# Performance work log

Hardware: AMD Instinct MI355X
Metric: run time of the kernel (lower is better)

## Reference

```python
import jax, jax.numpy as jnp
import numpy as np

INPUT_SIZE = 768
HIDDEN = [512, 256, 128]
LATENT = 32
NUM_LEVELS = 3
CODEBOOK_SIZE = 256
BATCH = 131072


def _init_linear(key, d_in, d_out):
    kw, kb = jax.random.split(key)
    lim = 1.0 / np.sqrt(d_in)
    W = jax.random.uniform(kw, (d_in, d_out), jnp.float32, -lim, lim)
    b = jax.random.uniform(kb, (d_out,), jnp.float32, -lim, lim)
    return W, b


def setup_inputs() -> dict:
    key = jax.random.key(0)
    keys = jax.random.split(key, 16)
    inp = {"x": jax.random.normal(keys[0], (BATCH, INPUT_SIZE), jnp.float32)}
    enc_dims = [INPUT_SIZE] + HIDDEN + [LATENT]          # 768->512->256->128->32
    dec_dims = [LATENT] + HIDDEN[::-1] + [INPUT_SIZE]     # 32->128->256->512->768
    for i in range(4):
        W, b = _init_linear(keys[1 + i], enc_dims[i], enc_dims[i + 1])
        inp[f"enc_W{i}"], inp[f"enc_b{i}"] = W, b
        W, b = _init_linear(keys[6 + i], dec_dims[i], dec_dims[i + 1])
        inp[f"dec_W{i}"], inp[f"dec_b{i}"] = W, b
    inp["codebooks"] = jax.random.normal(keys[12], (NUM_LEVELS, CODEBOOK_SIZE, LATENT), jnp.float32)
    return inp


def _mlp(x, Ws, bs):
    # Linear -> ReLU (-> Dropout p=0, identity) between layers, final layer linear.
    n = len(Ws)
    for i in range(n):
        x = x @ Ws[i] + bs[i]
        if i < n - 1:
            x = jax.nn.relu(x)
    return x


def _quantize(z, codebooks):
    # Residual vector quantization over NUM_LEVELS codebooks.
    L, K, D = codebooks.shape
    r = z
    idxs, rs, es = [], [], []
    for l in range(L):
        c = codebooks[l]                                  # [K, D]
        # squared-distance argmin (same argmin as cdist)
        d = jnp.sum(r * r, axis=-1, keepdims=True) - 2.0 * (r @ c.T) + jnp.sum(c * c, axis=-1)
        idx = jnp.argmin(d, axis=-1)                      # [B]
        e = c[idx]                                        # [B, D] gather
        idxs.append(idx)
        rs.append(r)
        es.append(e)
        r = r - e
    quantized = jnp.stack(idxs, axis=1)                   # [B, L] int codes
    r_stack = jnp.stack(rs, axis=1)                       # [B, L, D] residual inputs per level
    e_stack = jnp.stack(es, axis=1)                       # [B, L, D] selected embeddings
    sum_e = jnp.sum(e_stack, axis=1)                      # [B, D]
    # straight-through estimator
    z_hat = z + jax.lax.stop_gradient(sum_e - z)
    counts = jnp.sum(jax.nn.one_hot(quantized, K, dtype=jnp.float32), axis=0)  # [L, K] usage
    return quantized, r_stack, e_stack, z_hat, counts


def reference(x,
              enc_W0, enc_b0, enc_W1, enc_b1, enc_W2, enc_b2, enc_W3, enc_b3,
              dec_W0, dec_b0, dec_W1, dec_b1, dec_W2, dec_b2, dec_W3, dec_b3,
              codebooks):
    encoded = _mlp(x, [enc_W0, enc_W1, enc_W2, enc_W3], [enc_b0, enc_b1, enc_b2, enc_b3])
    quantized, r, e, z_hat, counts = _quantize(encoded, codebooks)
    decoded = _mlp(z_hat, [dec_W0, dec_W1, dec_W2, dec_W3], [dec_b0, dec_b1, dec_b2, dec_b3])
    return decoded, r, e, counts, quantized
```

## Files before the change

### kernel.cpp

```cpp
#include <hip/hip_runtime.h>
#include <hip/hip_bf16.h>
#include <cfloat>

#define B_TOTAL 131072
#define IN_DIM  768
#define NLEV    3
#define KCODE   256

typedef unsigned short u16;
typedef unsigned int   u32;
typedef __attribute__((ext_vector_type(8))) short bf16x8;
typedef __attribute__((ext_vector_type(4))) float f32x4;

#define GLOAD_LDS(g, l)                                                        \
    __builtin_amdgcn_global_load_lds(                                          \
        (const __attribute__((address_space(1))) u32*)(g),                     \
        (__attribute__((address_space(3))) u32*)(l), 16, 0, 0)

#define SWZ(row) ((((row) >> 1) & 3u) << 4)

__device__ __forceinline__ u16 f2bf(float x) {
    union { __hip_bfloat16 h; u16 u; } c;
    c.h = __float2bfloat16(x);
    return c.u;
}
__device__ __forceinline__ float bf2f(u32 lo16) {
    union { u32 v; float f; } c;
    c.v = lo16 << 16;
    return c.f;
}
__device__ __forceinline__ u32 pack2(float a, float b) {
    return (u32)f2bf(a) | ((u32)f2bf(b) << 16);
}

template<int K, int N, bool AF32, bool RELU, bool OUTF32>
__global__ __launch_bounds__(512)
void gemm_mfma(const void* __restrict__ A_, const u16* __restrict__ Wt,
               const float* __restrict__ bias, void* __restrict__ C_)
{
    constexpr int NK  = K / 32;
    constexpr int NCB = N / 128;
    __shared__ u16 As[3][8192];
    __shared__ u16 Bs[3][4096];

    const int tid  = threadIdx.x;
    const int lane = tid & 63;
    const int wid  = tid >> 6;
    const int wrow = wid >> 1;
    const int wcol = wid & 1;

    const u32 nwg  = gridDim.x;
    const u32 orig = blockIdx.x;
    const u32 xcd = orig & 7u, q8 = nwg >> 3, r8 = nwg & 7u;
    const u32 wg = (xcd < r8 ? xcd * (q8 + 1) : r8 * (q8 + 1) + (xcd - r8) * q8)
                 + (orig >> 3);
    const int col0 = (int)(wg % NCB) * 128;
    const int row0 = (int)(wg / NCB) * 256;

    const u16*   Ab = (const u16*)A_;
    const float* Af = (const float*)A_;

    f32x4 acc[4][4];
    #pragma unroll
    for (int i = 0; i < 4; ++i)
        #pragma unroll
        for (int j = 0; j < 4; ++j) acc[i][j] = (f32x4){0.f, 0.f, 0.f, 0.f};

    auto stage_B = [&](u16* dstbase, const u16* src) {
        const u32 o   = (u32)(tid * 16);
        const u32 row = o >> 6;
        const u32 cbs = (o & 63u) ^ SWZ(row);
        GLOAD_LDS((const char*)(src + (size_t)row * K) + cbs,
                  dstbase + wid * 512);
    };
    auto stage_A = [&](u16* dstbase, const u16* src) {
        #pragma unroll
        for (int i = 0; i < 2; ++i) {
            const u32 o   = (u32)(i * 8192 + tid * 16);
            const u32 row = o >> 6;
            const u32 cbs = (o & 63u) ^ SWZ(row);
            GLOAD_LDS((const char*)(src + (size_t)row * K) + cbs,
                      dstbase + (i * 4096 + wid * 512));
        }
    };
    auto stage_tile = [&](int buf, int kt) {
        stage_B(&Bs[buf][0], Wt + (size_t)col0 * K + kt * 32);
        stage_A(&As[buf][0], Ab + (size_t)row0 * K + kt * 32);
    };

    auto compute = [&](int buf) {
        const char* Ab8 = (const char*)&As[buf][0];
        const char* Bb8 = (const char*)&Bs[buf][0];
        const int kb = (lane >> 4) * 16;
        bf16x8 af[4], bf[4];
        #pragma unroll
        for (int mf = 0; mf < 4; ++mf) {
            const int r = wrow * 64 + mf * 16 + (lane & 15);
            af[mf] = *(const bf16x8*)(Ab8 + r * 64 + (kb ^ SWZ(r)));
        }
        #pragma unroll
        for (int nf = 0; nf < 4; ++nf) {
            const int r = wcol * 64 + nf * 16 + (lane & 15);
            bf[nf] = *(const bf16x8*)(Bb8 + r * 64 + (kb ^ SWZ(r)));
        }
        __builtin_amdgcn_s_setprio(1);
        #pragma unroll
        for (int mf = 0; mf < 4; ++mf)
            #pragma unroll
            for (int nf = 0; nf < 4; ++nf)
                acc[mf][nf] = __builtin_amdgcn_mfma_f32_16x16x32_bf16(
                    af[mf], bf[nf], acc[mf][nf], 0, 0, 0);
        __builtin_amdgcn_s_setprio(0);
    };

    if constexpr (AF32) {
        float4 fa[4];
        auto loadA = [&](int kt) {
            const int row = tid >> 1;
            const int ce0 = (tid & 1) * 16;
            const float* s = &Af[(size_t)(row0 + row) * K + kt * 32 + ce0];
            fa[0] = *(const float4*)(s + 0);
            fa[1] = *(const float4*)(s + 4);
            fa[2] = *(const float4*)(s + 8);
            fa[3] = *(const float4*)(s + 12);
        };
        auto writeA = [&](int buf) {
            const int row = tid >> 1;
            const u32 cb0 = (u32)((tid & 1) * 32);
            const u32 sw  = SWZ(row);
            char* lb = (char*)&As[buf][0] + row * 64;
            *(uint4*)(lb + ((cb0 + 0) ^ sw)) = make_uint4(
                pack2(fa[0].x, fa[0].y), pack2(fa[0].z, fa[0].w),
                pack2(fa[1].x, fa[1].y), pack2(fa[1].z, fa[1].w));
            *(uint4*)(lb + ((cb0 + 16) ^ sw)) = make_uint4(
                pack2(fa[2].x, fa[2].y), pack2(fa[2].z, fa[2].w),
                pack2(fa[3].x, fa[3].y), pack2(fa[3].z, fa[3].w));
        };

        loadA(0);
        stage_B(&Bs[0][0], Wt + (size_t)col0 * K);
        writeA(0);
        if (NK > 1) {
            loadA(1);
            stage_B(&Bs[1][0], Wt + (size_t)col0 * K + 32);
        }

        #pragma unroll 1
        for (int kt = 0; kt < NK; ++kt) {
            if (kt == NK - 1) asm volatile("s_waitcnt vmcnt(0) lgkmcnt(0)");
            else              asm volatile("s_waitcnt vmcnt(5) lgkmcnt(0)");
            __builtin_amdgcn_sched_barrier(0);
            __builtin_amdgcn_s_barrier();
            __builtin_amdgcn_sched_barrier(0);
            if (kt + 1 < NK) writeA((kt + 1) % 3);
            if (kt + 2 < NK) {
                loadA(kt + 2);
                stage_B(&Bs[(kt + 2) % 3][0],
                        Wt + (size_t)col0 * K + (kt + 2) * 32);
            }
            compute(kt % 3);
        }
    } else {
        stage_tile(0, 0);
        if (NK > 1) stage_tile(1, 1);
        int cb_ = 0, sb_ = 2;
        #pragma unroll 1
        for (int kt = 0; kt < NK; ++kt) {
            if (kt == NK - 1) asm volatile("s_waitcnt vmcnt(0)");
            else              asm volatile("s_waitcnt vmcnt(3)");
            __builtin_amdgcn_sched_barrier(0);
            __builtin_amdgcn_s_barrier();
            __builtin_amdgcn_sched_barrier(0);
            if (kt + 2 < NK) stage_tile(sb_, kt + 2);
            compute(cb_);
            cb_ = (cb_ == 2) ? 0 : cb_ + 1;
            sb_ = (sb_ == 2) ? 0 : sb_ + 1;
        }
    }

    #pragma unroll
    for (int nf = 0; nf < 4; ++nf) {
        const int col = col0 + wcol * 64 + nf * 16 + (lane & 15);
        const float bv = bias[col];
        #pragma unroll
        for (int mf = 0; mf < 4; ++mf) {
            const int rbase = row0 + wrow * 64 + mf * 16 + (lane >> 4) * 4;
            #pragma unroll
            for (int r = 0; r < 4; ++r) {
                float o = acc[mf][nf][r] + bv;
                if (RELU) o = fmaxf(o, 0.f);
                if constexpr (OUTF32)
                    ((float*)C_)[(size_t)(rbase + r) * N + col] = o;
                else
                    ((u16*)C_)[(size_t)(rbase + r) * N + col] = f2bf(o);
            }
        }
    }
}

template<int K, int N>
__global__ __launch_bounds__(256)
void wcvt(const float* __restrict__ W, u16* __restrict__ Wt)
{
    const int idx = blockIdx.x * 256 + threadIdx.x;
    const int k = idx / N, n = idx - k * N;
    Wt[(size_t)n * K + k] = f2bf(W[idx]);
}

__global__ __launch_bounds__(256)
void vq_kernel(const u16* __restrict__ h3, const float* __restrict__ eW3,
               const float* __restrict__ eb3, const float* __restrict__ cb,
               float* __restrict__ r_out, float* __restrict__ e_out,
               float* __restrict__ q_out, u16* __restrict__ se_ws,
               u32* __restrict__ ghist, size_t grow_base)
{
    __shared__ float W3[128 * 32];
    __shared__ float ebv[32];
    __shared__ float clds[256 * 36];
    __shared__ float cc2[256];
    __shared__ u32   lh[NLEV * KCODE];

    const int tid = threadIdx.x;
    const size_t lrow = (size_t)blockIdx.x * 256 + tid;
    const size_t grow = grow_base + lrow;

    for (int i = tid; i < 128 * 32; i += 256) W3[i] = eW3[i];
    if (tid < 32) ebv[tid] = eb3[tid];
    for (int i = tid; i < NLEV * KCODE; i += 256) lh[i] = 0;
    __syncthreads();

    float r[32];
    #pragma unroll
    for (int j = 0; j < 32; ++j) r[j] = ebv[j];
    {
        const u32* hrow = (const u32*)h3 + lrow * 64;
        #pragma unroll 2
        for (int k2 = 0; k2 < 64; ++k2) {
            const u32 v = hrow[k2];
            const float x0 = bf2f(v & 0xffffu), x1 = bf2f(v >> 16);
            const float* w0 = &W3[(2 * k2) * 32];
            const float* w1 = &W3[(2 * k2 + 1) * 32];
            #pragma unroll
            for (int j4 = 0; j4 < 8; ++j4) {
                const float4 a = *(const float4*)&w0[4 * j4];
                const float4 b = *(const float4*)&w1[4 * j4];
                r[4*j4+0] = fmaf(x1, b.x, fmaf(x0, a.x, r[4*j4+0]));
                r[4*j4+1] = fmaf(x1, b.y, fmaf(x0, a.y, r[4*j4+1]));
                r[4*j4+2] = fmaf(x1, b.z, fmaf(x0, a.z, r[4*j4+2]));
                r[4*j4+3] = fmaf(x1, b.w, fmaf(x0, a.w, r[4*j4+3]));
            }
        }
    }

    float z0[32];
    #pragma unroll
    for (int j = 0; j < 32; ++j) z0[j] = r[j];

    #pragma unroll 1
    for (int l = 0; l < NLEV; ++l) {
        __syncthreads();
        {
            const float* cl = cb + ((size_t)l * KCODE + tid) * 32;
            float s = 0.f;
            #pragma unroll
            for (int m = 0; m < 8; ++m) {
                const float4 v = *(const float4*)&cl[4 * m];
                *(float4*)&clds[tid * 36 + 4 * m] = v;
                s = fmaf(v.x, v.x, s); s = fmaf(v.y, v.y, s);
                s = fmaf(v.z, v.z, s); s = fmaf(v.w, v.w, s);
            }
            cc2[tid] = -0.5f * s;
        }
        __syncthreads();

        float best = -FLT_MAX;
        int   bidx = 0;
        #pragma unroll 1
        for (int k = 0; k < KCODE; ++k) {
            const float* ck = &clds[k * 36];
            float d0 = 0.f, d1 = 0.f, d2 = 0.f, d3 = 0.f;
            #pragma unroll
            for (int m = 0; m < 8; m += 4) {
                const float4 v0 = *(const float4*)&ck[4 * (m + 0)];
                const float4 v1 = *(const float4*)&ck[4 * (m + 1)];
                const float4 v2 = *(const float4*)&ck[4 * (m + 2)];
                const float4 v3 = *(const float4*)&ck[4 * (m + 3)];
                d0 = fmaf(r[4*m+0],  v0.x, d0); d0 = fmaf(r[4*m+1],  v0.y, d0);
                d0 = fmaf(r[4*m+2],  v0.z, d0); d0 = fmaf(r[4*m+3],  v0.w, d0);
                d1 = fmaf(r[4*m+4],  v1.x, d1); d1 = fmaf(r[4*m+5],  v1.y, d1);
                d1 = fmaf(r[4*m+6],  v1.z, d1); d1 = fmaf(r[4*m+7],  v1.w, d1);
                d2 = fmaf(r[4*m+8],  v2.x, d2); d2 = fmaf(r[4*m+9],  v2.y, d2);
                d2 = fmaf(r[4*m+10], v2.z, d2); d2 = fmaf(r[4*m+11], v2.w, d2);
                d3 = fmaf(r[4*m+12], v3.x, d3); d3 = fmaf(r[4*m+13], v3.y, d3);
                d3 = fmaf(r[4*m+14], v3.z, d3); d3 = fmaf(r[4*m+15], v3.w, d3);
            }
            const float s = ((d0 + d1) + (d2 + d3)) + cc2[k];
            if (s > best) { best = s; bidx = k; }
        }

        const size_t base = (grow * NLEV + l) * 32;
        const float* ce = &clds[bidx * 36];
        #pragma unroll
        for (int m = 0; m < 8; ++m) {
            const float4 ev = *(const float4*)&ce[4 * m];
            *(float4*)&r_out[base + 4 * m] =
                make_float4(r[4*m+0], r[4*m+1], r[4*m+2], r[4*m+3]);
            *(float4*)&e_out[base + 4 * m] = ev;
            r[4*m+0] -= ev.x; r[4*m+1] -= ev.y;
            r[4*m+2] -= ev.z; r[4*m+3] -= ev.w;
        }
        q_out[grow * NLEV + l] = (float)bidx;
        atomicAdd(&lh[l * KCODE + bidx], 1u);
    }

    u32* sed = (u32*)se_ws + lrow * 16;
    #pragma unroll
    for (int m = 0; m < 16; ++m)
        sed[m] = pack2(z0[2*m] - r[2*m], z0[2*m+1] - r[2*m+1]);

    __syncthreads();
    for (int i = tid; i < NLEV * KCODE; i += 256)
        if (lh[i]) atomicAdd(&ghist[i], lh[i]);
}

__global__ void zero_hist(u32* h) {
    if (threadIdx.x < NLEV * KCODE) h[threadIdx.x] = 0;
}
__global__ void counts_fin(const u32* __restrict__ g, float* __restrict__ o) {
    if (threadIdx.x < NLEV * KCODE) o[threadIdx.x] = (float)g[threadIdx.x];
}

__global__ __launch_bounds__(256)
void counts_k(const float* __restrict__ q, float* __restrict__ cnt)
{
    const int l = blockIdx.x >> 8;
    const int k = blockIdx.x & 255;
    const float pat = (float)k;
    int c = 0;
    for (int i = threadIdx.x; i < B_TOTAL; i += 256)
        c += (q[(size_t)i * NLEV + l] == pat) ? 1 : 0;
    __shared__ int red[256];
    red[threadIdx.x] = c;
    __syncthreads();
    for (int s = 128; s > 0; s >>= 1) {
        if (threadIdx.x < s) red[threadIdx.x] += red[threadIdx.x + s];
        __syncthreads();
    }
    if (threadIdx.x == 0)
        cnt[blockIdx.x] = (float)red[0];
}

template<int K, int N, bool RELU, bool AGLOBAL>
static __device__ __forceinline__
void layer16(const float* __restrict__ A, size_t grow0,
             const float* __restrict__ W, const float* __restrict__ bias,
             float* __restrict__ C)
{
    constexpr int QPT = N / 128;
    const int tr = threadIdx.x >> 5;
    const int tc = threadIdx.x & 31;
    float acc[2][QPT * 4];
    #pragma unroll
    for (int i = 0; i < 2; ++i)
        #pragma unroll
        for (int j = 0; j < QPT * 4; ++j) acc[i][j] = 0.f;
    #pragma unroll 2
    for (int k0 = 0; k0 < K; k0 += 4) {
        float4 av[2];
        #pragma unroll
        for (int i = 0; i < 2; ++i) {
            if (AGLOBAL)
                av[i] = *(const float4*)&A[(grow0 + tr * 2 + i) * (size_t)K + k0];
            else
                av[i] = *(const float4*)&A[(tr * 2 + i) * K + k0];
        }
        #pragma unroll
        for (int kk = 0; kk < 4; ++kk) {
            #pragma unroll
            for (int q = 0; q < QPT; ++q) {
                const float4 w4 = *(const float4*)&W[(size_t)(k0 + kk) * N + 4 * (tc + 32 * q)];
                #pragma unroll
                for (int i = 0; i < 2; ++i) {
                    const float a = ((const float*)&av[i])[kk];
                    acc[i][4*q+0] = fmaf(a, w4.x, acc[i][4*q+0]);
                    acc[i][4*q+1] = fmaf(a, w4.y, acc[i][4*q+1]);
                    acc[i][4*q+2] = fmaf(a, w4.z, acc[i][4*q+2]);
                    acc[i][4*q+3] = fmaf(a, w4.w, acc[i][4*q+3]);
                }
            }
        }
    }
    #pragma unroll
    for (int q = 0; q < QPT; ++q) {
        const float4 b4 = *(const float4*)&bias[4 * (tc + 32 * q)];
        #pragma unroll
        for (int i = 0; i < 2; ++i) {
            float4 o;
            o.x = acc[i][4*q+0] + b4.x; o.y = acc[i][4*q+1] + b4.y;
            o.z = acc[i][4*q+2] + b4.z; o.w = acc[i][4*q+3] + b4.w;
            if (RELU) {
                o.x = fmaxf(o.x, 0.f); o.y = fmaxf(o.y, 0.f);
                o.z = fmaxf(o.z, 0.f); o.w = fmaxf(o.w, 0.f);
            }
            *(float4*)&C[(tr * 2 + i) * N + 4 * (tc + 32 * q)] = o;
        }
    }
}

static __device__ __forceinline__
void layer_final16(const float* __restrict__ A, const float* __restrict__ W,
                   const float* __restrict__ bias, float* __restrict__ Cg, size_t grow0)
{
    constexpr int QPT = 6;
    const int tr = threadIdx.x >> 5;
    const int tc = threadIdx.x & 31;
    float acc[2][QPT * 4];
    #pragma unroll
    for (int i = 0; i < 2; ++i)
        #pragma unroll
        for (int j = 0; j < QPT * 4; ++j) acc[i][j] = 0.f;
    #pragma unroll 2
    for (int k0 = 0; k0 < 512; k0 += 4) {
        float4 av[2];
        #pragma unroll
        for (int i = 0; i < 2; ++i)
            av[i] = *(const float4*)&A[(tr * 2 + i) * 512 + k0];
        #pragma unroll
        for (int kk = 0; kk < 4; ++kk) {
            #pragma unroll
            for (int q = 0; q < QPT; ++q) {
                const float4 w4 = *(const float4*)&W[(size_t)(k0 + kk) * 768 + 4 * (tc + 32 * q)];
                #pragma unroll
                for (int i = 0; i < 2; ++i) {
                    const float a = ((const float*)&av[i])[kk];
                    acc[i][4*q+0] = fmaf(a, w4.x, acc[i][4*q+0]);
                    acc[i][4*q+1] = fmaf(a, w4.y, acc[i][4*q+1]);
                    acc[i][4*q+2] = fmaf(a, w4.z, acc[i][4*q+2]);
                    acc[i][4*q+3] = fmaf(a, w4.w, acc[i][4*q+3]);
                }
            }
        }
    }
    #pragma unroll
    for (int q = 0; q < QPT; ++q) {
        const float4 b4 = *(const float4*)&bias[4 * (tc + 32 * q)];
        #pragma unroll
        for (int i = 0; i < 2; ++i) {
            float4 s;
            s.x = acc[i][4*q+0] + b4.x; s.y = acc[i][4*q+1] + b4.y;
            s.z = acc[i][4*q+2] + b4.z; s.w = acc[i][4*q+3] + b4.w;
            *(float4*)&Cg[(grow0 + tr * 2 + i) * (size_t)768 + 4 * (tc + 32 * q)] = s;
        }
    }
}

static __device__ __forceinline__
void layer_narrow16(const float* __restrict__ A, const float* __restrict__ W,
                    const float* __restrict__ bias, float* __restrict__ Z)
{
    const int row = threadIdx.x >> 4;
    const int g   = threadIdx.x & 15;
    float a0 = 0.f, a1 = 0.f;
    #pragma unroll 4
    for (int k0 = 0; k0 < 128; k0 += 4) {
        const float4 av = *(const float4*)&A[row * 128 + k0];
        #pragma unroll
        for (int kk = 0; kk < 4; ++kk) {
            const float2 w2 = *(const float2*)&W[(k0 + kk) * 32 + 2 * g];
            const float a = ((const float*)&av)[kk];
            a0 = fmaf(a, w2.x, a0);
            a1 = fmaf(a, w2.y, a1);
        }
    }
    Z[row * 36 + 2 * g + 0] = a0 + bias[2 * g + 0];
    Z[row * 36 + 2 * g + 1] = a1 + bias[2 * g + 1];
}

__global__ __launch_bounds__(256)
void enc_vq_kernel(const float* __restrict__ x,
                   const float* __restrict__ eW0, const float* __restrict__ eb0,
                   const float* __restrict__ eW1, const float* __restrict__ eb1,
                   const float* __restrict__ eW2, const float* __restrict__ eb2,
                   const float* __restrict__ eW3, const float* __restrict__ eb3,
                   const float* __restrict__ cb,
                   float* __restrict__ r_out, float* __restrict__ e_out,
                   float* __restrict__ q_out)
{
    __shared__ __align__(16) char smem[59648];
    float* h1   = (float*)(smem);
    float* h2   = (float*)(smem + 32768);
    float* h3   = (float*)(smem + 49152);
    float* z    = (float*)(smem + 57344);
    float* clds = (float*)(smem);
    float* cc   = (float*)(smem + 36864);

    const size_t grow0 = (size_t)blockIdx.x * 16;
    layer16<768, 512, true, true >(x,  grow0, eW0, eb0, h1);
    __syncthreads();
    layer16<512, 256, true, false>(h1, 0,     eW1, eb1, h2);
    __syncthreads();
    layer16<256, 128, true, false>(h2, 0,     eW2, eb2, h3);
    __syncthreads();
    layer_narrow16(h3, eW3, eb3, z);

    const int row = threadIdx.x >> 4;
    const int g   = threadIdx.x & 15;
    const size_t grow = grow0 + row;

    #pragma unroll 1
    for (int l = 0; l < NLEV; ++l) {
        __syncthreads();
        {
            const float* cl = cb + (size_t)l * KCODE * 32;
            const int t = threadIdx.x;
            float s = 0.f;
            #pragma unroll
            for (int m = 0; m < 8; ++m) {
                const float4 v = *(const float4*)&cl[t * 32 + 4 * m];
                *(float4*)&clds[t * 36 + 4 * m] = v;
                s = fmaf(v.x, v.x, s); s = fmaf(v.y, v.y, s);
                s = fmaf(v.z, v.z, s); s = fmaf(v.w, v.w, s);
            }
            cc[t] = s;
        }
        __syncthreads();

        float r[32];
        #pragma unroll
        for (int m = 0; m < 8; ++m) {
            const float4 v = *(const float4*)&z[row * 36 + 4 * m];
            r[4*m+0] = v.x; r[4*m+1] = v.y; r[4*m+2] = v.z; r[4*m+3] = v.w;
        }
        float rr = 0.f;
        #pragma unroll
        for (int j = 0; j < 32; ++j) rr = fmaf(r[j], r[j], rr);

        float best = FLT_MAX;
        int   bidx = 0x7fffffff;
        #pragma unroll 1
        for (int t = 0; t < 16; ++t) {
            const int k = g + 16 * t;
            const float* ck = &clds[k * 36];
            float d0 = 0.f, d1 = 0.f, d2 = 0.f, d3 = 0.f;
            #pragma unroll
            for (int m = 0; m < 8; m += 4) {
                const float4 v0 = *(const float4*)&ck[4 * (m + 0)];
                const float4 v1 = *(const float4*)&ck[4 * (m + 1)];
                const float4 v2 = *(const float4*)&ck[4 * (m + 2)];
                const float4 v3 = *(const float4*)&ck[4 * (m + 3)];
                d0 = fmaf(r[4*m+0],  v0.x, d0); d0 = fmaf(r[4*m+1],  v0.y, d0);
                d0 = fmaf(r[4*m+2],  v0.z, d0); d0 = fmaf(r[4*m+3],  v0.w, d0);
                d1 = fmaf(r[4*m+4],  v1.x, d1); d1 = fmaf(r[4*m+5],  v1.y, d1);
                d1 = fmaf(r[4*m+6],  v1.z, d1); d1 = fmaf(r[4*m+7],  v1.w, d1);
                d2 = fmaf(r[4*m+8],  v2.x, d2); d2 = fmaf(r[4*m+9],  v2.y, d2);
                d2 = fmaf(r[4*m+10], v2.z, d2); d2 = fmaf(r[4*m+11], v2.w, d2);
                d3 = fmaf(r[4*m+12], v3.x, d3); d3 = fmaf(r[4*m+13], v3.y, d3);
                d3 = fmaf(r[4*m+14], v3.z, d3); d3 = fmaf(r[4*m+15], v3.w, d3);
            }
            const float dot = (d0 + d1) + (d2 + d3);
            const float d = (rr - 2.f * dot) + cc[k];
            if (d < best || (d == best && k < bidx)) { best = d; bidx = k; }
        }
        #pragma unroll
        for (int off = 1; off < 16; off <<= 1) {
            const float ob = __shfl_xor(best, off);
            const int   oi = __shfl_xor(bidx, off);
            if (ob < best || (ob == best && oi < bidx)) { best = ob; bidx = oi; }
        }

        const float evx = clds[bidx * 36 + 2 * g + 0];
        const float evy = clds[bidx * 36 + 2 * g + 1];
        *(float2*)&r_out[(grow * NLEV + l) * 32 + 2 * g] = make_float2(r[2*g], r[2*g+1]);
        *(float2*)&e_out[(grow * NLEV + l) * 32 + 2 * g] = make_float2(evx, evy);
        if (g == 0) q_out[grow * NLEV + l] = (float)bidx;
        z[row * 36 + 2 * g + 0] = r[2 * g + 0] - evx;
        z[row * 36 + 2 * g + 1] = r[2 * g + 1] - evy;
    }
}

__global__ __launch_bounds__(256)
void dec_kernel(const float* __restrict__ e_in,
                const float* __restrict__ dW0, const float* __restrict__ db0,
                const float* __restrict__ dW1, const float* __restrict__ db1,
                const float* __restrict__ dW2, const float* __restrict__ db2,
                const float* __restrict__ dW3, const float* __restrict__ db3,
                float* __restrict__ dec_out)
{
    __shared__ __align__(16) char smem[59392];
    float* h3 = (float*)(smem);
    float* h2 = (float*)(smem + 32768);
    float* h1 = (float*)(smem + 49152);
    float* se = (float*)(smem + 57344);

    const size_t grow0 = (size_t)blockIdx.x * 16;
    const int row = threadIdx.x >> 4;
    const int g   = threadIdx.x & 15;
    {
        const size_t base = ((grow0 + row) * NLEV) * 32 + 2 * g;
        float s0 = 0.f, s1 = 0.f;
        #pragma unroll
        for (int l = 0; l < NLEV; ++l) {
            const float2 v = *(const float2*)&e_in[base + l * 32];
            s0 += v.x; s1 += v.y;
        }
        se[row * 32 + 2 * g + 0] = s0;
        se[row * 32 + 2 * g + 1] = s1;
    }
    __syncthreads();
    layer16<32,  128, true, false>(se, 0, dW0, db0, h1);
    __syncthreads();
    layer16<128, 256, true, false>(h1, 0, dW1, db1, h2);
    __syncthreads();
    layer16<256, 512, true, false>(h2, 0, dW2, db2, h3);
    __syncthreads();
    layer_final16(h3, dW3, db3, dec_out, grow0);
}

extern "C" void kernel_launch(void* const* d_in, const int* in_sizes, int n_in,
                              void* d_out, int out_size, void* d_ws, size_t ws_size,
                              hipStream_t stream)
{
    (void)in_sizes; (void)n_in; (void)out_size;
    const float* x  = (const float*)d_in[0];
    const float* cb = (const float*)d_in[17];
    const float *eW[4], *eb[4], *dW[4], *db[4];
    for (int i = 0; i < 4; ++i) {
        eW[i] = (const float*)d_in[1 + 4 * i];
        eb[i] = (const float*)d_in[2 + 4 * i];
        dW[i] = (const float*)d_in[3 + 4 * i];
        db[i] = (const float*)d_in[4 + 4 * i];
    }

    float* out = (float*)d_out;
    const size_t OFF_R = (size_t)B_TOTAL * IN_DIM;
    const size_t OFF_E = OFF_R + (size_t)B_TOTAL * NLEV * 32;
    const size_t OFF_C = OFF_E + (size_t)B_TOTAL * NLEV * 32;
    const size_t OFF_Q = OFF_C + (size_t)NLEV * KCODE;

    const size_t WTB = 2236416;
    size_t R = 0;
    for (size_t cand = 131072; cand >= 2048; cand >>= 1)
        if (WTB + cand * 3648 + 4096 <= ws_size) { R = cand; break; }

    if (R && d_ws) {
        u16* Wp   = (u16*)d_ws;
        u16* WtE0 = Wp;
        u16* WtE1 = WtE0 + 393216;
        u16* WtE2 = WtE1 + 131072;
        u16* WtD0 = WtE2 + 32768;
        u16* WtD1 = WtD0 + 4096;
        u16* WtD2 = WtD1 + 32768;
        u16* WtD3 = WtD2 + 131072;
        u16* h1   = WtD3 + 393216;
        u16* h2   = h1 + R * 512;
        u16* h3   = h2 + R * 256;
        u16* se   = h3 + R * 128;
        u16* d1   = se + R * 32;
        u16* d2   = d1 + R * 128;
        u16* d3   = d2 + R * 256;
        u32* ghist = (u32*)(d3 + R * 512);

        wcvt<768, 512><<<dim3((768 * 512) / 256), 256, 0, stream>>>(eW[0], WtE0);
        wcvt<512, 256><<<dim3((512 * 256) / 256), 256, 0, stream>>>(eW[1], WtE1);
        wcvt<256, 128><<<dim3((256 * 128) / 256), 256, 0, stream>>>(eW[2], WtE2);
        wcvt<32,  128><<<dim3((32 * 128) / 256),  256, 0, stream>>>(dW[0], WtD0);
        wcvt<128, 256><<<dim3((128 * 256) / 256), 256, 0, stream>>>(dW[1], WtD1);
        wcvt<256, 512><<<dim3((256 * 512) / 256), 256, 0, stream>>>(dW[2], WtD2);
        wcvt<512, 768><<<dim3((512 * 768) / 256), 256, 0, stream>>>(dW[3], WtD3);
        zero_hist<<<1, 768, 0, stream>>>(ghist);

        const int nch = B_TOTAL / (int)R;
        const int MB2 = (int)R / 256;
        for (int c = 0; c < nch; ++c) {
            const size_t rb = (size_t)c * R;
            gemm_mfma<768, 512, true,  true,  false><<<dim3(4 * MB2), 512, 0, stream>>>(
                x + rb * 768, WtE0, eb[0], h1);
            gemm_mfma<512, 256, false, true,  false><<<dim3(2 * MB2), 512, 0, stream>>>(
                h1, WtE1, eb[1], h2);
            gemm_mfma<256, 128, false, true,  false><<<dim3(1 * MB2), 512, 0, stream>>>(
                h2, WtE2, eb[2], h3);
            vq_kernel<<<dim3((int)R / 256), 256, 0, stream>>>(
                h3, eW[3], eb[3], cb,
                out + OFF_R, out + OFF_E, out + OFF_Q, se, ghist, rb);
            gemm_mfma<32,  128, false, true,  false><<<dim3(1 * MB2), 512, 0, stream>>>(
                se, WtD0, db[0], d1);
            gemm_mfma<128, 256, false, true,  false><<<dim3(2 * MB2), 512, 0, stream>>>(
                d1, WtD1, db[1], d2);
            gemm_mfma<256, 512, false, true,  false><<<dim3(4 * MB2), 512, 0, stream>>>(
                d2, WtD2, db[2], d3);
            gemm_mfma<512, 768, false, false, true ><<<dim3(6 * MB2), 512, 0, stream>>>(
                d3, WtD3, db[3], out + rb * 768);
        }
        counts_fin<<<1, 768, 0, stream>>>(ghist, out + OFF_C);
    } else {
        enc_vq_kernel<<<dim3(B_TOTAL / 16), 256, 0, stream>>>(
            x, eW[0], eb[0], eW[1], eb[1], eW[2], eb[2], eW[3], eb[3], cb,
            out + OFF_R, out + OFF_E, out + OFF_Q);
        counts_k<<<dim3(NLEV * KCODE), 256, 0, stream>>>(out + OFF_Q, out + OFF_C);
        dec_kernel<<<dim3(B_TOTAL / 16), 256, 0, stream>>>(
            out + OFF_E, dW[0], db[0], dW[1], db[1], dW[2], db[2], dW[3], db[3], out);
    }
}
```

Before: 852.0 us.

## Add 256x256-tile MFMA GEMM for wide layers and merge weight prep kernels

Adds a GEMM variant with 256x256 output tiles (each wave computes 128x64) and uses it for the encoder 512->256 layer and the three wider decoder layers. This halves the block count and raises operand reuse per LDS load. It also merges the seven weight-transpose kernels and the histogram zeroing into one prep launch to cut launch overhead. The cost is higher register pressure (32 accumulators per lane) and fewer blocks per layer, which may reduce occupancy and tail balance.

New measurement: 878.3 us. 1.03x slower.

```diff
diff --git a/kernel.cpp b/kernel.cpp
--- a/kernel.cpp
+++ b/kernel.cpp
@@ -31,6 +31,12 @@
 }
 __device__ __forceinline__ u32 pack2(float a, float b) {
     return (u32)f2bf(a) | ((u32)f2bf(b) << 16);
+}
+
+__device__ __forceinline__ u32 xcd_swizzle(u32 orig, u32 nwg) {
+    const u32 xcd = orig & 7u, q8 = nwg >> 3, r8 = nwg & 7u;
+    return (xcd < r8 ? xcd * (q8 + 1) : r8 * (q8 + 1) + (xcd - r8) * q8)
+           + (orig >> 3);
 }
 
 template<int K, int N, bool AF32, bool RELU, bool OUTF32>
@@ -49,11 +55,7 @@
     const int wrow = wid >> 1;
     const int wcol = wid & 1;
 
-    const u32 nwg  = gridDim.x;
-    const u32 orig = blockIdx.x;
-    const u32 xcd = orig & 7u, q8 = nwg >> 3, r8 = nwg & 7u;
-    const u32 wg = (xcd < r8 ? xcd * (q8 + 1) : r8 * (q8 + 1) + (xcd - r8) * q8)
-                 + (orig >> 3);
+    const u32 wg = xcd_swizzle(blockIdx.x, gridDim.x);
     const int col0 = (int)(wg % NCB) * 128;
     const int row0 = (int)(wg / NCB) * 256;
 
@@ -198,13 +200,142 @@
     }
 }
 
-template<int K, int N>
+template<int K, int N, bool RELU, bool OUTF32>
+__global__ __launch_bounds__(512)
+void gemm_mfma256(const u16* __restrict__ Ab, const u16* __restrict__ Wt,
+                  const float* __restrict__ bias, void* __restrict__ C_)
+{
+    constexpr int NK  = K / 32;
+    constexpr int NCB = N / 256;
+    __shared__ u16 As[3][8192];
+    __shared__ u16 Bs[3][8192];
+
+    const int tid  = threadIdx.x;
+    const int lane = tid & 63;
+    const int wid  = tid >> 6;
+    const int wrow = wid >> 2;
+    const int wcol = wid & 3;
+
+    const u32 wg = xcd_swizzle(blockIdx.x, gridDim.x);
+    const int col0 = (int)(wg % NCB) * 256;
+    const int row0 = (int)(wg / NCB) * 256;
+
+    f32x4 acc[8][4];
+    #pragma unroll
+    for (int i = 0; i < 8; ++i)
+        #pragma unroll
+        for (int j = 0; j < 4; ++j) acc[i][j] = (f32x4){0.f, 0.f, 0.f, 0.f};
+
+    auto stage_one = [&](u16* dstbase, const u16* src) {
+        #pragma unroll
+        for (int i = 0; i < 2; ++i) {
+            const u32 o   = (u32)(i * 8192 + tid * 16);
+            const u32 row = o >> 6;
+            const u32 cbs = (o & 63u) ^ SWZ(row);
+            GLOAD_LDS((const char*)(src + (size_t)row * K) + cbs,
+                      dstbase + (i * 4096 + wid * 512));
+        }
+    };
+    auto stage_tile = [&](int buf, int kt) {
+        stage_one(&Bs[buf][0], Wt + (size_t)col0 * K + kt * 32);
+        stage_one(&As[buf][0], Ab + (size_t)row0 * K + kt * 32);
+    };
+
+    auto compute = [&](int buf) {
+        const char* Ab8 = (const char*)&As[buf][0];
+        const char* Bb8 = (const char*)&Bs[buf][0];
+        const int kb = (lane >> 4) * 16;
+        bf16x8 af[8], bf[4];
+        #pragma unroll
+        for (int mf = 0; mf < 8; ++mf) {
+            const int r = wrow * 128 + mf * 16 + (lane & 15);
+            af[mf] = *(const bf16x8*)(Ab8 + r * 64 + (kb ^ SWZ(r)));
+        }
+        #pragma unroll
+        for (int nf = 0; nf < 4; ++nf) {
+            const int r = wcol * 64 + nf * 16 + (lane & 15);
+            bf[nf] = *(const bf16x8*)(Bb8 + r * 64 + (kb ^ SWZ(r)));
+        }
+        __builtin_amdgcn_s_setprio(1);
+        #pragma unroll
+        for (int mf = 0; mf < 8; ++mf)
+            #pragma unroll
+            for (int nf = 0; nf < 4; ++nf)
+                acc[mf][nf] = __builtin_amdgcn_mfma_f32_16x16x32_bf16(
+                    af[mf], bf[nf], acc[mf][nf], 0, 0, 0);
+        __builtin_amdgcn_s_setprio(0);
+    };
+
+    stage_tile(0, 0);
+    if (NK > 1) stage_tile(1, 1);
+    int cb_ = 0, sb_ = 2;
+    #pragma unroll 1
+    for (int kt = 0; kt < NK; ++kt) {
+        if (kt == NK - 1) asm volatile("s_waitcnt vmcnt(0)");
+        else              asm volatile("s_waitcnt vmcnt(4)");
+        __builtin_amdgcn_sched_barrier(0);
+        __builtin_amdgcn_s_barrier();
+        __builtin_amdgcn_sched_barrier(0);
+        if (kt + 2 < NK) stage_tile(sb_, kt + 2);
+        compute(cb_);
+        cb_ = (cb_ == 2) ? 0 : cb_ + 1;
+        sb_ = (sb_ == 2) ? 0 : sb_ + 1;
+    }
+
+    #pragma unroll
+    for (int nf = 0; nf < 4; ++nf) {
+        const int col = col0 + wcol * 64 + nf * 16 + (lane & 15);
+        const float bv = bias[col];
+        #pragma unroll
+        for (int mf = 0; mf < 8; ++mf) {
+            const int rbase = row0 + wrow * 128 + mf * 16 + (lane >> 4) * 4;
+            #pragma unroll
+            for (int r = 0; r < 4; ++r) {
+                float o = acc[mf][nf][r] + bv;
+                if (RELU) o = fmaxf(o, 0.f);
+                if constexpr (OUTF32)
+                    ((float*)C_)[(size_t)(rbase + r) * N + col] = o;
+                else
+                    ((u16*)C_)[(size_t)(rbase + r) * N + col] = f2bf(o);
+            }
+        }
+    }
+}
+
 __global__ __launch_bounds__(256)
-void wcvt(const float* __restrict__ W, u16* __restrict__ Wt)
-{
-    const int idx = blockIdx.x * 256 + threadIdx.x;
-    const int k = idx / N, n = idx - k * N;
-    Wt[(size_t)n * K + k] = f2bf(W[idx]);
+void prep(const float* __restrict__ eW0, const float* __restrict__ eW1,
+          const float* __restrict__ eW2, const float* __restrict__ dW0,
+          const float* __restrict__ dW1, const float* __restrict__ dW2,
+          const float* __restrict__ dW3,
+          u16* __restrict__ tE0, u16* __restrict__ tE1, u16* __restrict__ tE2,
+          u16* __restrict__ tD0, u16* __restrict__ tD1, u16* __restrict__ tD2,
+          u16* __restrict__ tD3, u32* __restrict__ ghist)
+{
+    const int i = blockIdx.x * 256 + threadIdx.x;
+    if (i < 393216) {
+        const int k = i >> 9, n = i & 511;
+        tE0[(size_t)n * 768 + k] = f2bf(eW0[i]);
+    } else if (i < 524288) {
+        const int j = i - 393216, k = j >> 8, n = j & 255;
+        tE1[(size_t)n * 512 + k] = f2bf(eW1[j]);
+    } else if (i < 557056) {
+        const int j = i - 524288, k = j >> 7, n = j & 127;
+        tE2[(size_t)n * 256 + k] = f2bf(eW2[j]);
+    } else if (i < 561152) {
+        const int j = i - 557056, k = j >> 7, n = j & 127;
+        tD0[(size_t)n * 32 + k] = f2bf(dW0[j]);
+    } else if (i < 593920) {
+        const int j = i - 561152, k = j >> 8, n = j & 255;
+        tD1[(size_t)n * 128 + k] = f2bf(dW1[j]);
+    } else if (i < 724992) {
+        const int j = i - 593920, k = j >> 9, n = j & 511;
+        tD2[(size_t)n * 256 + k] = f2bf(dW2[j]);
+    } else if (i < 1118208) {
+        const int j = i - 724992, k = j / 768, n = j - k * 768;
+        tD3[(size_t)n * 512 + k] = f2bf(dW3[j]);
+    } else if (i < 1118976) {
+        ghist[i - 1118208] = 0;
+    }
 }
 
 __global__ __launch_bounds__(256)
@@ -323,9 +454,6 @@
         if (lh[i]) atomicAdd(&ghist[i], lh[i]);
 }
 
-__global__ void zero_hist(u32* h) {
-    if (threadIdx.x < NLEV * KCODE) h[threadIdx.x] = 0;
-}
 __global__ void counts_fin(const u32* __restrict__ g, float* __restrict__ o) {
     if (threadIdx.x < NLEV * KCODE) o[threadIdx.x] = (float)g[threadIdx.x];
 }
@@ -660,14 +788,9 @@
         u16* d3   = d2 + R * 256;
         u32* ghist = (u32*)(d3 + R * 512);
 
-        wcvt<768, 512><<<dim3((768 * 512) / 256), 256, 0, stream>>>(eW[0], WtE0);
-        wcvt<512, 256><<<dim3((512 * 256) / 256), 256, 0, stream>>>(eW[1], WtE1);
-        wcvt<256, 128><<<dim3((256 * 128) / 256), 256, 0, stream>>>(eW[2], WtE2);
-        wcvt<32,  128><<<dim3((32 * 128) / 256),  256, 0, stream>>>(dW[0], WtD0);
-        wcvt<128, 256><<<dim3((128 * 256) / 256), 256, 0, stream>>>(dW[1], WtD1);
-        wcvt<256, 512><<<dim3((256 * 512) / 256), 256, 0, stream>>>(dW[2], WtD2);
-        wcvt<512, 768><<<dim3((512 * 768) / 256), 256, 0, stream>>>(dW[3], WtD3);
-        zero_hist<<<1, 768, 0, stream>>>(ghist);
+        prep<<<dim3(4371), 256, 0, stream>>>(
+            eW[0], eW[1], eW[2], dW[0], dW[1], dW[2], dW[3],
+            WtE0, WtE1, WtE2, WtD0, WtD1, WtD2, WtD3, ghist);
 
         const int nch = B_TOTAL / (int)R;
         const int MB2 = (int)R / 256;
@@ -675,7 +798,7 @@
             const size_t rb = (size_t)c * R;
             gemm_mfma<768, 512, true,  true,  false><<<dim3(4 * MB2), 512, 0, stream>>>(
                 x + rb * 768, WtE0, eb[0], h1);
-            gemm_mfma<512, 256, false, true,  false><<<dim3(2 * MB2), 512, 0, stream>>>(
+            gemm_mfma256<512, 256, true, false><<<dim3(1 * MB2), 512, 0, stream>>>(
                 h1, WtE1, eb[1], h2);
             gemm_mfma<256, 128, false, true,  false><<<dim3(1 * MB2), 512, 0, stream>>>(
                 h2, WtE2, eb[2], h3);
@@ -684,11 +807,11 @@
                 out + OFF_R, out + OFF_E, out + OFF_Q, se, ghist, rb);
             gemm_mfma<32,  128, false, true,  false><<<dim3(1 * MB2), 512, 0, stream>>>(
                 se, WtD0, db[0], d1);
-            gemm_mfma<128, 256, false, true,  false><<<dim3(2 * MB2), 512, 0, stream>>>(
+            gemm_mfma256<128, 256, true, false><<<dim3(1 * MB2), 512, 0, stream>>>(
                 d1, WtD1, db[1], d2);
-            gemm_mfma<256, 512, false, true,  false><<<dim3(4 * MB2), 512, 0, stream>>>(
+            gemm_mfma256<256, 512, true, false><<<dim3(2 * MB2), 512, 0, stream>>>(
                 d2, WtD2, db[2], d3);
-            gemm_mfma<512, 768, false, false, true ><<<dim3(6 * MB2), 512, 0, stream>>>(
+            gemm_mfma256<512, 768, false, true><<<dim3(3 * MB2), 512, 0, stream>>>(
                 d3, WtD3, db[3], out + rb * 768);
         }
         counts_fin<<<1, 768, 0, stream>>>(ghist, out + OFF_C);
```
